# Kernel tuning notes

Measured on AMD Instinct MI355X. Metric: run time of the kernel, lower is better.

Reference implementation:

```python
import jax, jax.numpy as jnp
import numpy as np

TEMPERATURE = 0.1
NUM_CLASSES = 100


def setup_inputs() -> dict:
    key = jax.random.key(0)
    k1, k2 = jax.random.split(key)
    embeddings = jax.random.normal(k1, (8192, 128), dtype=jnp.float32)
    labels = jax.random.randint(k2, (8192,), 0, NUM_CLASSES, dtype=jnp.int64)
    return {"embeddings": embeddings, "labels": labels}


def reference(embeddings, labels):
    # L2-normalize rows (eps matches torch.nn.functional.normalize clamp)
    norm = jnp.maximum(jnp.linalg.norm(embeddings, axis=1, keepdims=True), 1e-12)
    e = embeddings / norm
    sim = jnp.matmul(e, e.T) / TEMPERATURE  # [N, N]
    n = sim.shape[0]
    eye = jnp.eye(n, dtype=bool)
    # positives: same label, excluding self
    pos = (labels[None, :] == labels[:, None]) & ~eye
    # The per-row torch loop computes soft-target cross-entropy over all
    # non-diagonal entries: row_loss_i = -sum_{j in pos(i)} log_softmax(sim[i, j!=i])_j.
    # log_softmax is permutation-invariant, so concatenation order is irrelevant.
    neg_inf = jnp.finfo(sim.dtype).min
    masked = jnp.where(eye, neg_inf, sim)
    logz = jax.nn.logsumexp(masked, axis=1, keepdims=True)  # [N, 1]
    logp = sim - logz  # [N, N]
    row_loss = -jnp.sum(jnp.where(pos, logp, 0.0), axis=1)  # rows with no positives contribute 0
    return jnp.sum(row_loss) / n
```

## Files before the change

### kernel.cpp

```cpp
#include <hip/hip_runtime.h>


#define N 8192
#define D 128
#define JSPLIT 32
#define IBLK 256
#define K2E 14.4269504088896340736f

typedef __bf16 bf16x8 __attribute__((ext_vector_type(8)));
typedef float f32x4 __attribute__((ext_vector_type(4)));

#define EBF_OFF  0
#define C_OFF    2097152
#define CNT_OFF  2148352
#define Z_OFF    2148864
#define ZERO_SZ  (51200 + 512 + 32768)

__device__ __forceinline__ unsigned short f32_to_bf16_rne(float f) {
    unsigned int u = __float_as_uint(f);
    u += 0x7fffu + ((u >> 16) & 1u);
    return (unsigned short)(u >> 16);
}

__device__ __forceinline__ float fast_exp2(float x) {
#if __has_builtin(__builtin_amdgcn_exp2f)
    return __builtin_amdgcn_exp2f(x);
#else
    return exp2f(x);
#endif
}

__device__ __forceinline__ float fast_log2(float x) {
#if __has_builtin(__builtin_amdgcn_logf)
    return __builtin_amdgcn_logf(x);
#else
    return log2f(x);
#endif
}


__global__ __launch_bounds__(256) void prep_kernel(
        const float* __restrict__ emb, const int* __restrict__ labels,
        unsigned char* __restrict__ ebf, float* __restrict__ C,
        int* __restrict__ cnt) {
    const int wave = threadIdx.x >> 6;
    const int lane = threadIdx.x & 63;
    const int row  = blockIdx.x * 4 + wave;

    const float2 v = *(const float2*)(emb + (size_t)row * D + lane * 2);
    float ss = v.x * v.x + v.y * v.y;
    #pragma unroll
    for (int off = 32; off; off >>= 1) ss += __shfl_xor(ss, off);
    const float inv = 1.0f / fmaxf(sqrtf(ss), 1e-12f);

    const int grp = row >> 4, col = row & 15;
    const int c = lane >> 4, q = (lane >> 2) & 3, j2 = lane & 3;
    unsigned int packed = (unsigned int)f32_to_bf16_rne(v.x * inv) |
                          ((unsigned int)f32_to_bf16_rne(v.y * inv) << 16);
    *(unsigned int*)(ebf + grp * 4096 + c * 1024 + q * 256 + col * 16 + j2 * 4) = packed;

    const int lab = labels[row];
    const int e0  = (lane * 2 + row * 2) & (D - 1);
    const float2 w2 = *(const float2*)(emb + (size_t)row * D + e0);
    atomicAdd(&C[lab * D + e0],     w2.x * inv);
    atomicAdd(&C[lab * D + e0 + 1], w2.y * inv);
    if (lane == 0) atomicAdd(&cnt[lab], 1);
}

__global__ __launch_bounds__(256) void zsum_kernel(
        const unsigned char* __restrict__ ebf, float* __restrict__ z) {
    const int t    = threadIdx.x;
    const int w    = t >> 6;
    const int lane = t & 63;
    const int q    = lane >> 4;
    const int col  = lane & 15;
    const int iw   = blockIdx.x * IBLK + w * 64;
    const int jb   = blockIdx.y * (N / JSPLIT);

    bf16x8 a[4][4];
    #pragma unroll
    for (int g = 0; g < 4; ++g) {
        const unsigned char* ag = ebf + (size_t)(iw / 16 + g) * 4096 + lane * 16;
        #pragma unroll
        for (int c = 0; c < 4; ++c) a[g][c] = *(const bf16x8*)(ag + c * 1024);
    }

    float zacc[4][4] = {{0.f,0.f,0.f,0.f},{0.f,0.f,0.f,0.f},
                        {0.f,0.f,0.f,0.f},{0.f,0.f,0.f,0.f}};

    #pragma unroll 4
    for (int jt = 0; jt < (N / JSPLIT) / 16; ++jt) {
        const int js = jb + jt * 16;
        const unsigned char* bg = ebf + (size_t)(js / 16) * 4096 + lane * 16;
        bf16x8 b[4];
        #pragma unroll
        for (int c = 0; c < 4; ++c) b[c] = *(const bf16x8*)(bg + c * 1024);

        #pragma unroll
        for (int g = 0; g < 4; ++g) {
            f32x4 acc = {0.f, 0.f, 0.f, 0.f};
            #pragma unroll
            for (int c = 0; c < 4; ++c)
                acc = __builtin_amdgcn_mfma_f32_16x16x32_bf16(a[g][c], b[c], acc, 0, 0, 0);
            if (js == iw + g * 16) {
                #pragma unroll
                for (int r = 0; r < 4; ++r)
                    zacc[g][r] += (col == q * 4 + r)
                        ? 0.0f : fast_exp2(fmaf(acc[r], K2E, -K2E));
            } else {
                #pragma unroll
                for (int r = 0; r < 4; ++r)
                    zacc[g][r] += fast_exp2(fmaf(acc[r], K2E, -K2E));
            }
        }
    }

    #pragma unroll
    for (int g = 0; g < 4; ++g)
        #pragma unroll
        for (int r = 0; r < 4; ++r) {
            float zv = zacc[g][r];
            zv += __shfl_xor(zv, 1);
            zv += __shfl_xor(zv, 2);
            zv += __shfl_xor(zv, 4);
            zv += __shfl_xor(zv, 8);
            if (col == 0) atomicAdd(&z[iw + g * 16 + q * 4 + r], zv);
        }
}

__global__ __launch_bounds__(256) void final_kernel(
        const float* __restrict__ emb, const int* __restrict__ labels,
        const float* __restrict__ C, const int* __restrict__ cnt,
        const float* __restrict__ z, float* __restrict__ out) {
    __shared__ float part[4];
    const int wave = threadIdx.x >> 6;
    const int lane = threadIdx.x & 63;

    float wsum = 0.0f;
    #pragma unroll
    for (int r = 0; r < 4; ++r) {
        const int row = blockIdx.x * 16 + wave * 4 + r;
        const int lab = labels[row];
        const float2 v  = *(const float2*)(emb + (size_t)row * D + lane * 2);
        const float2 c2 = *(const float2*)(C   + (size_t)lab * D + lane * 2);
        float ss = v.x * v.x + v.y * v.y;
        float d  = v.x * c2.x + v.y * c2.y;
        #pragma unroll
        for (int off = 32; off; off >>= 1) {
            ss += __shfl_xor(ss, off);
            d  += __shfl_xor(d,  off);
        }
        if (lane == 0) {
            const int P = cnt[lab] - 1;
            if (P > 0) {
                const float inv  = 1.0f / fmaxf(sqrtf(ss), 1e-12f);
                const float logz = 10.0f + 0.69314718056f * fast_log2(z[row]);
                const float S    = (d * inv) * 10.0f - 10.0f;
                wsum += (float)P * logz - S;
            }
        }
    }
    if (lane == 0) part[wave] = wsum;
    __syncthreads();
    if (threadIdx.x == 0) {
        const float tt = part[0] + part[1] + part[2] + part[3];
        atomicAdd(out, tt * (1.0f / (float)N));
    }
}

extern "C" void kernel_launch(void* const* d_in, const int* in_sizes, int n_in,
                              void* d_out, int out_size, void* d_ws, size_t ws_size,
                              hipStream_t stream) {
    const float* emb  = (const float*)d_in[0];
    const int* labels = (const int*)d_in[1];
    float* out        = (float*)d_out;
    char* ws          = (char*)d_ws;

    unsigned char* ebf = (unsigned char*)(ws + EBF_OFF);
    float* C           = (float*)(ws + C_OFF);
    int*   cnt         = (int*)(ws + CNT_OFF);
    float* z           = (float*)(ws + Z_OFF);

    hipMemsetAsync(ws + C_OFF, 0, ZERO_SZ, stream);
    hipMemsetAsync(d_out, 0, sizeof(float), stream);

    prep_kernel<<<N / 4, 256, 0, stream>>>(emb, labels, ebf, C, cnt);
    zsum_kernel<<<dim3(N / IBLK, JSPLIT), 256, 0, stream>>>(ebf, z);
    final_kernel<<<N / 16, 256, 0, stream>>>(emb, labels, C, cnt, z, out);
}
```

Measured before the change: 134.0 us.

## Shrink zsum row tile to one 16-row group per wave for higher occupancy

Each wave in the similarity/logsumexp kernel now handles a single 16-row group instead of four, and the row block shrinks from 256 to 64 rows. A launch-bounds hint asks for 8 blocks per CU. This cuts register use and raises occupancy and grid size, so memory latency should hide better. In exchange, every loaded B tile feeds only 4 MFMAs instead of 16, which raises global/L2 load traffic per unit of compute.

```diff
diff --git a/kernel.cpp b/kernel.cpp
--- a/kernel.cpp
+++ b/kernel.cpp
@@ -4,7 +4,8 @@
 #define N 8192
 #define D 128
 #define JSPLIT 32
-#define IBLK 256
+#define IBLK 64
+#define NT   ((N / JSPLIT) / 16)
 #define K2E 14.4269504088896340736f
 
 typedef __bf16 bf16x8 __attribute__((ext_vector_type(8)));
@@ -67,65 +68,60 @@
     if (lane == 0) atomicAdd(&cnt[lab], 1);
 }
 
-__global__ __launch_bounds__(256) void zsum_kernel(
+__global__ __launch_bounds__(256, 8) void zsum_kernel(
         const unsigned char* __restrict__ ebf, float* __restrict__ z) {
     const int t    = threadIdx.x;
     const int w    = t >> 6;
     const int lane = t & 63;
     const int q    = lane >> 4;
     const int col  = lane & 15;
-    const int iw   = blockIdx.x * IBLK + w * 64;
+    const int iw   = blockIdx.x * IBLK + w * 16;
     const int jb   = blockIdx.y * (N / JSPLIT);
 
-    bf16x8 a[4][4];
-    #pragma unroll
-    for (int g = 0; g < 4; ++g) {
-        const unsigned char* ag = ebf + (size_t)(iw / 16 + g) * 4096 + lane * 16;
+    bf16x8 a[4];
+    {
+        const unsigned char* ag = ebf + (size_t)(iw >> 4) * 4096 + lane * 16;
         #pragma unroll
-        for (int c = 0; c < 4; ++c) a[g][c] = *(const bf16x8*)(ag + c * 1024);
+        for (int c = 0; c < 4; ++c) a[c] = *(const bf16x8*)(ag + c * 1024);
     }
 
-    float zacc[4][4] = {{0.f,0.f,0.f,0.f},{0.f,0.f,0.f,0.f},
-                        {0.f,0.f,0.f,0.f},{0.f,0.f,0.f,0.f}};
+    float zacc[4] = {0.f, 0.f, 0.f, 0.f};
+    const unsigned char* bp = ebf + (size_t)(jb >> 4) * 4096 + lane * 16;
 
     #pragma unroll 4
-    for (int jt = 0; jt < (N / JSPLIT) / 16; ++jt) {
-        const int js = jb + jt * 16;
-        const unsigned char* bg = ebf + (size_t)(js / 16) * 4096 + lane * 16;
+    for (int jt = 0; jt < NT; ++jt) {
+        const unsigned char* np = bp + (size_t)jt * 4096;
         bf16x8 b[4];
         #pragma unroll
-        for (int c = 0; c < 4; ++c) b[c] = *(const bf16x8*)(bg + c * 1024);
+        for (int c = 0; c < 4; ++c) b[c] = *(const bf16x8*)(np + c * 1024);
 
+        f32x4 acc = {0.f, 0.f, 0.f, 0.f};
         #pragma unroll
-        for (int g = 0; g < 4; ++g) {
-            f32x4 acc = {0.f, 0.f, 0.f, 0.f};
+        for (int c = 0; c < 4; ++c)
+            acc = __builtin_amdgcn_mfma_f32_16x16x32_bf16(a[c], b[c], acc, 0, 0, 0);
+
+        const int js = jb + jt * 16;
+        if (js == iw) {
             #pragma unroll
-            for (int c = 0; c < 4; ++c)
-                acc = __builtin_amdgcn_mfma_f32_16x16x32_bf16(a[g][c], b[c], acc, 0, 0, 0);
-            if (js == iw + g * 16) {
-                #pragma unroll
-                for (int r = 0; r < 4; ++r)
-                    zacc[g][r] += (col == q * 4 + r)
-                        ? 0.0f : fast_exp2(fmaf(acc[r], K2E, -K2E));
-            } else {
-                #pragma unroll
-                for (int r = 0; r < 4; ++r)
-                    zacc[g][r] += fast_exp2(fmaf(acc[r], K2E, -K2E));
-            }
+            for (int r = 0; r < 4; ++r)
+                zacc[r] += (col == q * 4 + r)
+                    ? 0.0f : fast_exp2(fmaf(acc[r], K2E, -K2E));
+        } else {
+            #pragma unroll
+            for (int r = 0; r < 4; ++r)
+                zacc[r] += fast_exp2(fmaf(acc[r], K2E, -K2E));
         }
     }
 
     #pragma unroll
-    for (int g = 0; g < 4; ++g)
-        #pragma unroll
-        for (int r = 0; r < 4; ++r) {
-            float zv = zacc[g][r];
-            zv += __shfl_xor(zv, 1);
-            zv += __shfl_xor(zv, 2);
-            zv += __shfl_xor(zv, 4);
-            zv += __shfl_xor(zv, 8);
-            if (col == 0) atomicAdd(&z[iw + g * 16 + q * 4 + r], zv);
-        }
+    for (int r = 0; r < 4; ++r) {
+        float zv = zacc[r];
+        zv += __shfl_xor(zv, 1);
+        zv += __shfl_xor(zv, 2);
+        zv += __shfl_xor(zv, 4);
+        zv += __shfl_xor(zv, 8);
+        if (col == 0) atomicAdd(&z[iw + q * 4 + r], zv);
+    }
 }
 
 __global__ __launch_bounds__(256) void final_kernel(
```

After: 138.1 us. +3.0%, slower.
